# Performance work log

Hardware: AMD Instinct MI355X
Metric: run time of the kernel (lower is better)

Reference implementation:

```python
import jax, jax.numpy as jnp
import numpy as np

EPS = 1e-6                                   # VN leaky-relu denominator eps
BN_SCALE = np.float32(1.0 / np.sqrt(1.0 + 1e-5))  # eval-mode BatchNorm with default stats
NEG = 0.2                                    # negative_slope


def vn_lin(x, w):
    # x: [n, c, 3, ...]; w: [c, o] -> [n, o, 3, ...]
    return jnp.einsum('nc...,co->no...', x, w)


def vn_act(p, d):
    # Vector-Neuron leaky ReLU: project p off the half-space defined by direction d.
    dot = jnp.sum(p * d, axis=2, keepdims=True)
    dsq = jnp.sum(d * d, axis=2, keepdims=True)
    corr = p - (dot / (dsq + EPS)) * d
    return NEG * p + (1.0 - NEG) * jnp.where(dot >= 0, p, corr)


def score_net(x, w_vn, wd_vn, w_h1, w_h2, b_h2, temp=1.0):
    # CorrelationNet: VNLinearLeakyReLU(3 -> 2*ks) -> norm -> 1x1 convs -> softmax
    p = vn_lin(x, w_vn) * BN_SCALE           # [N, 2ks, 3, K] (VNBatchNorm ~ scalar in eval)
    d = vn_lin(x, wd_vn)
    s = vn_act(p, d)
    s = jnp.linalg.norm(s, axis=2)           # [N, 2ks, K]
    s = jax.nn.relu(jnp.einsum('nck,co->nok', s, w_h1) * BN_SCALE)  # conv1d k=1, BN, relu
    s = jnp.einsum('nck,co->nok', s, w_h2) + b_h2[None, :, None]     # last conv with bias
    return jax.nn.softmax(s / temp, axis=1)  # [N, ks, K]


def setup_inputs() -> dict:
    key = jax.random.key(0)
    k = [jax.random.fold_in(key, i) for i in range(13)]
    N, N2, K, KS, OUT = 16000, 20000, 16, 8, 64
    half = OUT // 2
    return {
        'q_pts': jax.random.normal(k[0], (N, 3), jnp.float32),
        's_pts': jax.random.normal(k[1], (N2, 3), jnp.float32),
        's_feats': jax.random.normal(k[2], (N2, 1, 3), jnp.float32),
        'neighbor_indices': jax.random.randint(k[3], (N, K), 0, N2),
        'wb': jax.random.normal(k[4], (3, KS * half), jnp.float32) * np.float32(np.sqrt(2.0 / 3.0)),
        'w_vn': jax.random.normal(k[5], (3, 2 * KS), jnp.float32) * 0.5,
        'wd_vn': jax.random.normal(k[6], (3, 2 * KS), jnp.float32) * 0.5,
        'w_h1': jax.random.normal(k[7], (2 * KS, KS), jnp.float32) * 0.25,
        'w_h2': jax.random.normal(k[8], (KS, KS), jnp.float32) * 0.35,
        'b_h2': jnp.zeros((KS,), jnp.float32),
        'wd_relu': jax.random.normal(k[9], (half, half), jnp.float32) * 0.18,
        'w_un': jax.random.normal(k[10], (half, OUT), jnp.float32) * 0.18,
        'wd_un': jax.random.normal(k[11], (half, OUT), jnp.float32) * 0.18,
    }


def reference(q_pts, s_pts, s_feats, neighbor_indices, wb, w_vn, wd_vn,
              w_h1, w_h2, b_h2, wd_relu, w_un, wd_un):
    N, K = neighbor_indices.shape
    KS = w_h2.shape[1]
    # neighbor gather + centering: [N, K, 3] -> [N, 1, 3, K]
    pts = s_pts[neighbor_indices] - q_pts[:, None]
    pts = jnp.transpose(pts, (0, 2, 1))[:, None]
    centers = jnp.broadcast_to(jnp.mean(pts, axis=-1, keepdims=True), pts.shape)
    cross = jnp.cross(pts, centers, axis=2)
    local = jnp.concatenate([pts, centers, cross], axis=1)   # [N, 3, 3, K]
    scores = score_net(local, w_vn, wd_vn, w_h1, w_h2, b_h2)  # [N, KS, K]
    # kernel-point correlation conv
    pro = jnp.einsum('ncdk,cf->nfdk', local, wb)              # [N, KS*half, 3, K]
    pro = pro.reshape(N, KS, -1, 3, K)
    pro = jnp.sum(pro * scores[:, :, None, None, :], axis=1)  # [N, half, 3, K]
    nrm = jnp.linalg.norm(pro, axis=2, keepdims=True)
    normed = pro / jnp.maximum(nrm, 1e-12)                    # F.normalize(p=2, dim=2)
    feats = jnp.mean(normed, axis=-1)                         # [N, half, 3]
    feats = vn_act(feats, vn_lin(feats, wd_relu))             # VNLeakyReLU
    out = vn_act(vn_lin(feats, w_un) * BN_SCALE, vn_lin(feats, wd_un))  # VNLinearLeakyReLU
    return out                                                # [N, out_dim, 3]
```

## Files before the change

### kernel.cpp

```cpp
#include <hip/hip_runtime.h>
#include <math.h>

#define VN_EPS   1e-6f
#define NEG      0.2f
#define POS      0.8f

typedef float v2f __attribute__((ext_vector_type(2)));
typedef float v4f __attribute__((ext_vector_type(4)));

template <int CTRL>
__device__ __forceinline__ float dpp_add(float v) {
    int s = __builtin_amdgcn_update_dpp(0, __float_as_int(v), CTRL, 0xf, 0xf, true);
    return v + __int_as_float(s);
}
__device__ __forceinline__ float row16_allsum(float v) {
    v = dpp_add<0x128>(v);
    v = dpp_add<0x124>(v);
    v = dpp_add<0x122>(v);
    v = dpp_add<0x121>(v);
    return v;
}
__device__ __forceinline__ float row16_sum15(float v) {
    v = dpp_add<0x118>(v);
    v = dpp_add<0x114>(v);
    v = dpp_add<0x112>(v);
    v = dpp_add<0x111>(v);
    return v;
}

__global__ __launch_bounds__(256, 4) void areconv_kernel(
    const float* __restrict__ q_pts,
    const float* __restrict__ s_pts,
    const int*   __restrict__ nbr,
    const float* __restrict__ wb,
    const float* __restrict__ w_vn,
    const float* __restrict__ wd_vn,
    const float* __restrict__ w_h1,
    const float* __restrict__ w_h2,
    const float* __restrict__ b_h2,
    const float* __restrict__ wd_relu,
    const float* __restrict__ w_un,
    const float* __restrict__ wd_un,
    float* __restrict__ out,
    int N)
{
    const float BN_SCALE = 0.999994993f;

    __shared__ float featsA [4][3][36];
    __shared__ float feats2A[4][3][36];

    const int tid  = threadIdx.x;
    const int wv   = tid >> 6;
    const int lane = tid & 63;
    const int g    = (tid >> 4) & 3;
    const int k    = tid & 15;
    const int n    = blockIdx.x * 4 + wv;
    if (n >= N) return;

    const float qx = q_pts[n * 3 + 0];
    const float qy = q_pts[n * 3 + 1];
    const float qz = q_pts[n * 3 + 2];
    const int   id = nbr[n * 16 + k];
    const float px = s_pts[id * 3 + 0] - qx;
    const float py = s_pts[id * 3 + 1] - qy;
    const float pz = s_pts[id * 3 + 2] - qz;

    const float cx = row16_allsum(px) * 0.0625f;
    const float cy = row16_allsum(py) * 0.0625f;
    const float cz = row16_allsum(pz) * 0.0625f;

    const float rx = py * cz - pz * cy;
    const float ry = pz * cx - px * cz;
    const float rz = px * cy - py * cx;

    const float L[3][3] = {{px, py, pz}, {cx, cy, cz}, {rx, ry, rz}};

    float sn_loc[4];
#pragma unroll
    for (int j = 0; j < 4; ++j) {
        const int o = g * 4 + j;
        const float wv0 = w_vn[o],  wv1 = w_vn[16 + o],  wv2 = w_vn[32 + o];
        const float wd0 = wd_vn[o], wd1 = wd_vn[16 + o], wd2 = wd_vn[32 + o];
        float pv[3], dv[3];
        float dot = 0.f, dsq = 0.f;
#pragma unroll
        for (int d = 0; d < 3; ++d) {
            const float pp = BN_SCALE * (L[0][d] * wv0 + L[1][d] * wv1 + L[2][d] * wv2);
            const float dd = L[0][d] * wd0 + L[1][d] * wd1 + L[2][d] * wd2;
            pv[d] = pp; dv[d] = dd;
            dot += pp * dd;
            dsq += dd * dd;
        }
        const float f = dot * __builtin_amdgcn_rcpf(dsq + VN_EPS);
        float acc = 0.f;
#pragma unroll
        for (int d = 0; d < 3; ++d) {
            const float corr = pv[d] - f * dv[d];
            const float sel  = (dot >= 0.f) ? pv[d] : corr;
            const float a    = NEG * pv[d] + POS * sel;
            acc += a * a;
        }
        sn_loc[j] = __builtin_amdgcn_sqrtf(acc);
    }

    float tt[8];
#pragma unroll
    for (int op = 0; op < 4; ++op) {
        v2f t = sn_loc[0] * (*(const v2f*)&w_h1[(g * 4 + 0) * 8 + 2 * op])
              + sn_loc[1] * (*(const v2f*)&w_h1[(g * 4 + 1) * 8 + 2 * op])
              + sn_loc[2] * (*(const v2f*)&w_h1[(g * 4 + 2) * 8 + 2 * op])
              + sn_loc[3] * (*(const v2f*)&w_h1[(g * 4 + 3) * 8 + 2 * op]);
        float t0 = t[0], t1 = t[1];
        t0 += __shfl_xor(t0, 16);  t0 += __shfl_xor(t0, 32);
        t1 += __shfl_xor(t1, 16);  t1 += __shfl_xor(t1, 32);
        tt[2 * op + 0] = fmaxf(t0 * BN_SCALE, 0.f);
        tt[2 * op + 1] = fmaxf(t1 * BN_SCALE, 0.f);
    }

    float sc[8];
    float mx = -1e30f;
#pragma unroll
    for (int op = 0; op < 4; ++op) {
        v2f u = *(const v2f*)&b_h2[2 * op];
#pragma unroll
        for (int c = 0; c < 8; ++c)
            u += tt[c] * (*(const v2f*)&w_h2[c * 8 + 2 * op]);
        sc[2 * op + 0] = u[0];
        sc[2 * op + 1] = u[1];
        mx = fmaxf(mx, fmaxf(u[0], u[1]));
    }
    float se = 0.f;
#pragma unroll
    for (int o = 0; o < 8; ++o) { sc[o] = __expf(sc[o] - mx); se += sc[o]; }
    const float inv_se = __builtin_amdgcn_rcpf(se);
#pragma unroll
    for (int o = 0; o < 8; ++o) sc[o] *= inv_se;

#pragma unroll
    for (int pg = 0; pg < 2; ++pg) {
        const int hb = g * 8 + pg * 4;
        v4f W0 = sc[0] * (*(const v4f*)&wb[0 * 256 + hb]);
        v4f W1 = sc[0] * (*(const v4f*)&wb[1 * 256 + hb]);
        v4f W2 = sc[0] * (*(const v4f*)&wb[2 * 256 + hb]);
#pragma unroll
        for (int s = 1; s < 8; ++s) {
            const float sv = sc[s];
            W0 += sv * (*(const v4f*)&wb[0 * 256 + s * 32 + hb]);
            W1 += sv * (*(const v4f*)&wb[1 * 256 + s * 32 + hb]);
            W2 += sv * (*(const v4f*)&wb[2 * 256 + s * 32 + hb]);
        }
        v4f V0 = L[0][0] * W0 + L[1][0] * W1 + L[2][0] * W2;
        v4f V1 = L[0][1] * W0 + L[1][1] * W1 + L[2][1] * W2;
        v4f V2 = L[0][2] * W0 + L[1][2] * W1 + L[2][2] * W2;
        v4f vv = V0 * V0 + V1 * V1 + V2 * V2;
        v4f inn;
#pragma unroll
        for (int e = 0; e < 4; ++e)
            inn[e] = __builtin_amdgcn_rsqf(fmaxf(vv[e], 1e-24f)) * 0.0625f;
        V0 *= inn; V1 *= inn; V2 *= inn;
        v4f X0, X1, X2;
#pragma unroll
        for (int e = 0; e < 4; ++e) {
            X0[e] = row16_sum15(V0[e]);
            X1[e] = row16_sum15(V1[e]);
            X2[e] = row16_sum15(V2[e]);
        }
        if (k == 15) {
            *(v4f*)&featsA[wv][0][hb] = X0;
            *(v4f*)&featsA[wv][1][hb] = X1;
            *(v4f*)&featsA[wv][2][hb] = X2;
        }
    }

    {
        const int o    = lane >> 1;
        const int half = lane & 1;
        v4f a0 = {0.f, 0.f, 0.f, 0.f}, a1 = a0, a2 = a0;
#pragma unroll
        for (int grp = 0; grp < 4; ++grp) {
            const int hb = half * 16 + grp * 4;
            const v4f w4 = { wd_relu[(hb + 0) * 32 + o], wd_relu[(hb + 1) * 32 + o],
                             wd_relu[(hb + 2) * 32 + o], wd_relu[(hb + 3) * 32 + o] };
            a0 += (*(const v4f*)&featsA[wv][0][hb]) * w4;
            a1 += (*(const v4f*)&featsA[wv][1][hb]) * w4;
            a2 += (*(const v4f*)&featsA[wv][2][hb]) * w4;
        }
        float d0 = a0[0] + a0[1] + a0[2] + a0[3];
        float d1 = a1[0] + a1[1] + a1[2] + a1[3];
        float d2 = a2[0] + a2[1] + a2[2] + a2[3];
        d0 += __shfl_xor(d0, 1);
        d1 += __shfl_xor(d1, 1);
        d2 += __shfl_xor(d2, 1);
        const float p0 = featsA[wv][0][o];
        const float p1 = featsA[wv][1][o];
        const float p2 = featsA[wv][2][o];
        const float dot = p0 * d0 + p1 * d1 + p2 * d2;
        const float dsq = d0 * d0 + d1 * d1 + d2 * d2;
        const float f   = dot * __builtin_amdgcn_rcpf(dsq + VN_EPS);
        const bool  pos = (dot >= 0.f);
        if (half == 0) {
            feats2A[wv][0][o] = NEG * p0 + POS * (pos ? p0 : (p0 - f * d0));
            feats2A[wv][1][o] = NEG * p1 + POS * (pos ? p1 : (p1 - f * d1));
            feats2A[wv][2][o] = NEG * p2 + POS * (pos ? p2 : (p2 - f * d2));
        }
    }

    {
        const int o = lane;
        v4f au0 = {0.f, 0.f, 0.f, 0.f}, au1 = au0, au2 = au0;
        v4f av0 = au0, av1 = au0, av2 = au0;
#pragma unroll
        for (int grp = 0; grp < 8; ++grp) {
            const int hb = grp * 4;
            const v4f f0 = *(const v4f*)&feats2A[wv][0][hb];
            const v4f f1 = *(const v4f*)&feats2A[wv][1][hb];
            const v4f f2 = *(const v4f*)&feats2A[wv][2][hb];
            const v4f wu = { w_un[(hb + 0) * 64 + o], w_un[(hb + 1) * 64 + o],
                             w_un[(hb + 2) * 64 + o], w_un[(hb + 3) * 64 + o] };
            const v4f wd = { wd_un[(hb + 0) * 64 + o], wd_un[(hb + 1) * 64 + o],
                             wd_un[(hb + 2) * 64 + o], wd_un[(hb + 3) * 64 + o] };
            au0 += f0 * wu; au1 += f1 * wu; au2 += f2 * wu;
            av0 += f0 * wd; av1 += f1 * wd; av2 += f2 * wd;
        }
        float u0 = (au0[0] + au0[1] + au0[2] + au0[3]) * BN_SCALE;
        float u1 = (au1[0] + au1[1] + au1[2] + au1[3]) * BN_SCALE;
        float u2 = (au2[0] + au2[1] + au2[2] + au2[3]) * BN_SCALE;
        float v0 = av0[0] + av0[1] + av0[2] + av0[3];
        float v1 = av1[0] + av1[1] + av1[2] + av1[3];
        float v2 = av2[0] + av2[1] + av2[2] + av2[3];
        const float dot = u0 * v0 + u1 * v1 + u2 * v2;
        const float dsq = v0 * v0 + v1 * v1 + v2 * v2;
        const float f   = dot * __builtin_amdgcn_rcpf(dsq + VN_EPS);
        const bool  pos = (dot >= 0.f);
        const long  base = (long)n * 192 + o * 3;
        out[base + 0] = NEG * u0 + POS * (pos ? u0 : (u0 - f * v0));
        out[base + 1] = NEG * u1 + POS * (pos ? u1 : (u1 - f * v1));
        out[base + 2] = NEG * u2 + POS * (pos ? u2 : (u2 - f * v2));
    }
}

extern "C" void kernel_launch(void* const* d_in, const int* in_sizes, int n_in,
                              void* d_out, int out_size, void* d_ws, size_t ws_size,
                              hipStream_t stream) {
    const float* q_pts   = (const float*)d_in[0];
    const float* s_pts   = (const float*)d_in[1];
    const int*   nbr     = (const int*)  d_in[3];
    const float* wb      = (const float*)d_in[4];
    const float* w_vn    = (const float*)d_in[5];
    const float* wd_vn   = (const float*)d_in[6];
    const float* w_h1    = (const float*)d_in[7];
    const float* w_h2    = (const float*)d_in[8];
    const float* b_h2    = (const float*)d_in[9];
    const float* wd_relu = (const float*)d_in[10];
    const float* w_un    = (const float*)d_in[11];
    const float* wd_un   = (const float*)d_in[12];
    float* out = (float*)d_out;

    const int N = in_sizes[0] / 3;
    const int blocks = (N + 3) / 4;
    areconv_kernel<<<blocks, 256, 0, stream>>>(
        q_pts, s_pts, nbr, wb, w_vn, wd_vn, w_h1, w_h2, b_h2,
        wd_relu, w_un, wd_un, out, N);
}
```

Baseline: 127.2 us.

## Map four points per wavefront with sixteen lanes each instead of one

Each 64-thread block now handles four query points. Sixteen lanes, one per neighbor, serve each point, and each lane computes all channels itself. Before, one wavefront per point split its channels across four lane groups, and every group redid the neighbor gather and local-frame setup. The change removes that duplicated gather and the cross-group shuffles in the score MLP. In exchange each lane does more work per stage and holds more registers (16 score values, larger loops), which may lower occupancy.

```diff
diff --git a/kernel.cpp b/kernel.cpp
--- a/kernel.cpp
+++ b/kernel.cpp
@@ -28,7 +28,11 @@
     return v;
 }
 
-__global__ __launch_bounds__(256, 4) void areconv_kernel(
+__device__ __forceinline__ float hsum4(v4f a) {
+    return (a[0] + a[1]) + (a[2] + a[3]);
+}
+
+__global__ __launch_bounds__(64, 4) void areconv_kernel(
     const float* __restrict__ q_pts,
     const float* __restrict__ s_pts,
     const int*   __restrict__ nbr,
@@ -49,13 +53,11 @@
     __shared__ float featsA [4][3][36];
     __shared__ float feats2A[4][3][36];
 
-    const int tid  = threadIdx.x;
-    const int wv   = tid >> 6;
-    const int lane = tid & 63;
-    const int g    = (tid >> 4) & 3;
-    const int k    = tid & 15;
-    const int n    = blockIdx.x * 4 + wv;
-    if (n >= N) return;
+    const int lane = threadIdx.x & 63;
+    const int p    = lane >> 4;
+    const int k    = lane & 15;
+    int n = blockIdx.x * 4 + p;
+    n = (n < N) ? n : (N - 1);
 
     const float qx = q_pts[n * 3 + 0];
     const float qy = q_pts[n * 3 + 1];
@@ -75,10 +77,9 @@
 
     const float L[3][3] = {{px, py, pz}, {cx, cy, cz}, {rx, ry, rz}};
 
-    float sn_loc[4];
-#pragma unroll
-    for (int j = 0; j < 4; ++j) {
-        const int o = g * 4 + j;
+    float sn[16];
+#pragma unroll
+    for (int o = 0; o < 16; ++o) {
         const float wv0 = w_vn[o],  wv1 = w_vn[16 + o],  wv2 = w_vn[32 + o];
         const float wd0 = wd_vn[o], wd1 = wd_vn[16 + o], wd2 = wd_vn[32 + o];
         float pv[3], dv[3];
@@ -100,21 +101,18 @@
             const float a    = NEG * pv[d] + POS * sel;
             acc += a * a;
         }
-        sn_loc[j] = __builtin_amdgcn_sqrtf(acc);
+        sn[o] = __builtin_amdgcn_sqrtf(acc);
     }
 
     float tt[8];
 #pragma unroll
     for (int op = 0; op < 4; ++op) {
-        v2f t = sn_loc[0] * (*(const v2f*)&w_h1[(g * 4 + 0) * 8 + 2 * op])
-              + sn_loc[1] * (*(const v2f*)&w_h1[(g * 4 + 1) * 8 + 2 * op])
-              + sn_loc[2] * (*(const v2f*)&w_h1[(g * 4 + 2) * 8 + 2 * op])
-              + sn_loc[3] * (*(const v2f*)&w_h1[(g * 4 + 3) * 8 + 2 * op]);
-        float t0 = t[0], t1 = t[1];
-        t0 += __shfl_xor(t0, 16);  t0 += __shfl_xor(t0, 32);
-        t1 += __shfl_xor(t1, 16);  t1 += __shfl_xor(t1, 32);
-        tt[2 * op + 0] = fmaxf(t0 * BN_SCALE, 0.f);
-        tt[2 * op + 1] = fmaxf(t1 * BN_SCALE, 0.f);
+        v2f t = {0.f, 0.f};
+#pragma unroll
+        for (int c = 0; c < 16; ++c)
+            t += sn[c] * (*(const v2f*)&w_h1[c * 8 + 2 * op]);
+        tt[2 * op + 0] = fmaxf(t[0] * BN_SCALE, 0.f);
+        tt[2 * op + 1] = fmaxf(t[1] * BN_SCALE, 0.f);
     }
 
     float sc[8];
@@ -137,8 +135,8 @@
     for (int o = 0; o < 8; ++o) sc[o] *= inv_se;
 
 #pragma unroll
-    for (int pg = 0; pg < 2; ++pg) {
-        const int hb = g * 8 + pg * 4;
+    for (int grp = 0; grp < 8; ++grp) {
+        const int hb = grp * 4;
         v4f W0 = sc[0] * (*(const v4f*)&wb[0 * 256 + hb]);
         v4f W1 = sc[0] * (*(const v4f*)&wb[1 * 256 + hb]);
         v4f W2 = sc[0] * (*(const v4f*)&wb[2 * 256 + hb]);
@@ -166,55 +164,62 @@
             X2[e] = row16_sum15(V2[e]);
         }
         if (k == 15) {
-            *(v4f*)&featsA[wv][0][hb] = X0;
-            *(v4f*)&featsA[wv][1][hb] = X1;
-            *(v4f*)&featsA[wv][2][hb] = X2;
+            *(v4f*)&featsA[p][0][hb] = X0;
+            *(v4f*)&featsA[p][1][hb] = X1;
+            *(v4f*)&featsA[p][2][hb] = X2;
         }
     }
 
     {
-        const int o    = lane >> 1;
-        const int half = lane & 1;
-        v4f a0 = {0.f, 0.f, 0.f, 0.f}, a1 = a0, a2 = a0;
-#pragma unroll
-        for (int grp = 0; grp < 4; ++grp) {
-            const int hb = half * 16 + grp * 4;
-            const v4f w4 = { wd_relu[(hb + 0) * 32 + o], wd_relu[(hb + 1) * 32 + o],
-                             wd_relu[(hb + 2) * 32 + o], wd_relu[(hb + 3) * 32 + o] };
-            a0 += (*(const v4f*)&featsA[wv][0][hb]) * w4;
-            a1 += (*(const v4f*)&featsA[wv][1][hb]) * w4;
-            a2 += (*(const v4f*)&featsA[wv][2][hb]) * w4;
-        }
-        float d0 = a0[0] + a0[1] + a0[2] + a0[3];
-        float d1 = a1[0] + a1[1] + a1[2] + a1[3];
-        float d2 = a2[0] + a2[1] + a2[2] + a2[3];
-        d0 += __shfl_xor(d0, 1);
-        d1 += __shfl_xor(d1, 1);
-        d2 += __shfl_xor(d2, 1);
-        const float p0 = featsA[wv][0][o];
-        const float p1 = featsA[wv][1][o];
-        const float p2 = featsA[wv][2][o];
-        const float dot = p0 * d0 + p1 * d1 + p2 * d2;
-        const float dsq = d0 * d0 + d1 * d1 + d2 * d2;
-        const float f   = dot * __builtin_amdgcn_rcpf(dsq + VN_EPS);
-        const bool  pos = (dot >= 0.f);
-        if (half == 0) {
-            feats2A[wv][0][o] = NEG * p0 + POS * (pos ? p0 : (p0 - f * d0));
-            feats2A[wv][1][o] = NEG * p1 + POS * (pos ? p1 : (p1 - f * d1));
-            feats2A[wv][2][o] = NEG * p2 + POS * (pos ? p2 : (p2 - f * d2));
-        }
-    }
-
-    {
-        const int o = lane;
-        v4f au0 = {0.f, 0.f, 0.f, 0.f}, au1 = au0, au2 = au0;
-        v4f av0 = au0, av1 = au0, av2 = au0;
+        v4f a0[2], a1[2], a2[2];
+#pragma unroll
+        for (int j = 0; j < 2; ++j) { a0[j] = (v4f)0.f; a1[j] = (v4f)0.f; a2[j] = (v4f)0.f; }
 #pragma unroll
         for (int grp = 0; grp < 8; ++grp) {
             const int hb = grp * 4;
-            const v4f f0 = *(const v4f*)&feats2A[wv][0][hb];
-            const v4f f1 = *(const v4f*)&feats2A[wv][1][hb];
-            const v4f f2 = *(const v4f*)&feats2A[wv][2][hb];
+            const v4f f0 = *(const v4f*)&featsA[p][0][hb];
+            const v4f f1 = *(const v4f*)&featsA[p][1][hb];
+            const v4f f2 = *(const v4f*)&featsA[p][2][hb];
+#pragma unroll
+            for (int j = 0; j < 2; ++j) {
+                const int o = k + 16 * j;
+                const v4f w4 = { wd_relu[(hb + 0) * 32 + o], wd_relu[(hb + 1) * 32 + o],
+                                 wd_relu[(hb + 2) * 32 + o], wd_relu[(hb + 3) * 32 + o] };
+                a0[j] += f0 * w4;
+                a1[j] += f1 * w4;
+                a2[j] += f2 * w4;
+            }
+        }
+#pragma unroll
+        for (int j = 0; j < 2; ++j) {
+            const int o = k + 16 * j;
+            const float d0 = hsum4(a0[j]);
+            const float d1 = hsum4(a1[j]);
+            const float d2 = hsum4(a2[j]);
+            const float p0 = featsA[p][0][o];
+            const float p1 = featsA[p][1][o];
+            const float p2 = featsA[p][2][o];
+            const float dot = p0 * d0 + p1 * d1 + p2 * d2;
+            const float dsq = d0 * d0 + d1 * d1 + d2 * d2;
+            const float f   = dot * __builtin_amdgcn_rcpf(dsq + VN_EPS);
+            const bool  pos = (dot >= 0.f);
+            feats2A[p][0][o] = NEG * p0 + POS * (pos ? p0 : (p0 - f * d0));
+            feats2A[p][1][o] = NEG * p1 + POS * (pos ? p1 : (p1 - f * d1));
+            feats2A[p][2][o] = NEG * p2 + POS * (pos ? p2 : (p2 - f * d2));
+        }
+    }
+
+#pragma unroll
+    for (int j = 0; j < 4; ++j) {
+        const int o = k + 16 * j;
+        v4f au0 = (v4f)0.f, au1 = (v4f)0.f, au2 = (v4f)0.f;
+        v4f av0 = (v4f)0.f, av1 = (v4f)0.f, av2 = (v4f)0.f;
+#pragma unroll
+        for (int grp = 0; grp < 8; ++grp) {
+            const int hb = grp * 4;
+            const v4f f0 = *(const v4f*)&feats2A[p][0][hb];
+            const v4f f1 = *(const v4f*)&feats2A[p][1][hb];
+            const v4f f2 = *(const v4f*)&feats2A[p][2][hb];
             const v4f wu = { w_un[(hb + 0) * 64 + o], w_un[(hb + 1) * 64 + o],
                              w_un[(hb + 2) * 64 + o], w_un[(hb + 3) * 64 + o] };
             const v4f wd = { wd_un[(hb + 0) * 64 + o], wd_un[(hb + 1) * 64 + o],
@@ -222,12 +227,12 @@
             au0 += f0 * wu; au1 += f1 * wu; au2 += f2 * wu;
             av0 += f0 * wd; av1 += f1 * wd; av2 += f2 * wd;
         }
-        float u0 = (au0[0] + au0[1] + au0[2] + au0[3]) * BN_SCALE;
-        float u1 = (au1[0] + au1[1] + au1[2] + au1[3]) * BN_SCALE;
-        float u2 = (au2[0] + au2[1] + au2[2] + au2[3]) * BN_SCALE;
-        float v0 = av0[0] + av0[1] + av0[2] + av0[3];
-        float v1 = av1[0] + av1[1] + av1[2] + av1[3];
-        float v2 = av2[0] + av2[1] + av2[2] + av2[3];
+        float u0 = hsum4(au0) * BN_SCALE;
+        float u1 = hsum4(au1) * BN_SCALE;
+        float u2 = hsum4(au2) * BN_SCALE;
+        float v0 = hsum4(av0);
+        float v1 = hsum4(av1);
+        float v2 = hsum4(av2);
         const float dot = u0 * v0 + u1 * v1 + u2 * v2;
         const float dsq = v0 * v0 + v1 * v1 + v2 * v2;
         const float f   = dot * __builtin_amdgcn_rcpf(dsq + VN_EPS);
@@ -258,7 +263,7 @@
 
     const int N = in_sizes[0] / 3;
     const int blocks = (N + 3) / 4;
-    areconv_kernel<<<blocks, 256, 0, stream>>>(
+    areconv_kernel<<<blocks, 64, 0, stream>>>(
         q_pts, s_pts, nbr, wb, w_vn, wd_vn, w_h1, w_h2, b_h2,
         wd_relu, w_un, wd_un, out, N);
 }
```

Result: faster. 108.7 us (-14.5%).
